# Performance work log

Hardware: AMD Instinct MI355X
Metric: run time of the kernel (lower is better)

The kernel has to match this reference:

```python
import jax, jax.numpy as jnp
import numpy as np

N, F, H, O, L, E = 20000, 256, 256, 128, 3, 320000


def setup_inputs() -> dict:
    key = jax.random.key(0)
    ks = jax.random.split(key, 8)
    x = jax.random.normal(ks[0], (N, F), dtype=jnp.float32)
    edge_index = jax.random.randint(ks[1], (2, E), 0, N, dtype=jnp.int64)
    edge_attributes = jax.random.uniform(ks[2], (E,), dtype=jnp.float32)
    s = 1.0 / np.sqrt(H)
    w_rel = jax.random.uniform(ks[3], (L, H, H), minval=-s, maxval=s, dtype=jnp.float32)
    b_rel = jax.random.uniform(ks[4], (L, H), minval=-s, maxval=s, dtype=jnp.float32)
    w_root = jax.random.uniform(ks[5], (L, H, H), minval=-s, maxval=s, dtype=jnp.float32)
    w_out = jax.random.uniform(ks[6], (H, O), minval=-s, maxval=s, dtype=jnp.float32)
    b_out = jax.random.uniform(ks[7], (O,), minval=-s, maxval=s, dtype=jnp.float32)
    return {"x": x, "edge_index": edge_index, "edge_attributes": edge_attributes,
            "w_rel": w_rel, "b_rel": b_rel, "w_root": w_root,
            "w_out": w_out, "b_out": b_out}


def reference(x, edge_index, edge_attributes, w_rel, b_rel, w_root, w_out, b_out):
    # PyG GraphConv: h_i' = W_root h_i + W_rel (sum_{j->i} e_ji h_j) + b_rel
    src = edge_index[0]  # message source j
    dst = edge_index[1]  # message target i
    n = x.shape[0]
    h = x
    for l in range(w_rel.shape[0]):
        msgs = h[src] * edge_attributes[:, None]            # [E, H] gather + scale
        agg = jax.ops.segment_sum(msgs, dst, num_segments=n)  # [N, H] scatter-add
        h = jax.nn.relu(agg @ w_rel[l] + b_rel[l] + h @ w_root[l])
    return jax.nn.relu(h @ w_out + b_out)  # [N, O]
```

## Files before the change

kernel.cpp:

```cpp
#include <hip/hip_runtime.h>

#define NREAL 20000
#define MPAD  20096
#define HDIM  256
#define ODIM  128
#define NEDGE 320000
#define SCAN_B 20

typedef __attribute__((ext_vector_type(4))) float f32x4;
typedef __attribute__((ext_vector_type(2))) float f32x2;
typedef __attribute__((ext_vector_type(8))) short s16x8;
typedef __attribute__((ext_vector_type(4))) unsigned short u16x4;
typedef unsigned short u16;
typedef unsigned int u32;

__device__ inline u16 f2bf(float f) {
    u32 u = __float_as_uint(f);
    return (u16)((u + 0x7FFFu + ((u >> 16) & 1u)) >> 16);
}
__device__ inline float bf2f(u16 s) { return __uint_as_float(((u32)s) << 16); }

__device__ __forceinline__ void gload16(const void* g, void* l) {
    __builtin_amdgcn_global_load_lds((const __attribute__((address_space(1))) void*)g,
                                     (__attribute__((address_space(3))) void*)l, 16, 0, 0);
}

__global__ __launch_bounds__(256) void k_prep(
    const float* __restrict__ x, u16* __restrict__ hbf,
    const float* __restrict__ wrel, const float* __restrict__ wroot,
    const float* __restrict__ wout,
    u16* __restrict__ brelT, u16* __restrict__ brootT, u16* __restrict__ boutT,
    const int* __restrict__ dst, int* __restrict__ deg)
{
    const int gt = blockIdx.x * 256 + threadIdx.x;
    const int gsz = gridDim.x * 256;
    for (long gid = gt; gid < (long)MPAD * HDIM / 4; gid += gsz) {
        long base = gid * 4;
        long row  = base >> 8;
        f32x4 v = {0.f, 0.f, 0.f, 0.f};
        if (row < NREAL) v = *(const f32x4*)(x + base);
        u16x4 hv;
        for (int j = 0; j < 4; ++j) hv[j] = f2bf(v[j]);
        *(u16x4*)(hbf + base) = hv;
    }
    for (int i = gt; i < 3 * 65536; i += gsz) {
        int l = i >> 16, r = i & 65535, n = r >> 8, k = r & 255;
        brelT[i]  = f2bf(wrel [l * 65536 + k * 256 + n]);
        brootT[i] = f2bf(wroot[l * 65536 + k * 256 + n]);
    }
    for (int i = gt; i < 128 * 256; i += gsz) {
        int n = i >> 8, k = i & 255;
        boutT[i] = f2bf(wout[k * 128 + n]);
    }
    for (int e = gt; e < NEDGE; e += gsz) atomicAdd(&deg[dst[e]], 1);
}

__global__ __launch_bounds__(1024) void k_blocksum(const int* __restrict__ deg,
                                                   int* __restrict__ bsum) {
    __shared__ int red[16];
    int b = blockIdx.x, t = threadIdx.x;
    int i = b * 1024 + t;
    int v = (i < NREAL) ? deg[i] : 0;
    for (int off = 32; off; off >>= 1) v += __shfl_down(v, off);
    if ((t & 63) == 0) red[t >> 6] = v;
    __syncthreads();
    if (t < 16) {
        int s = red[t];
        for (int off = 8; off; off >>= 1) s += __shfl_down(s, off);
        if (t == 0) bsum[b] = s;
    }
}

__global__ void k_scansmall(const int* __restrict__ bsum, int* __restrict__ boff) {
    int t = threadIdx.x;
    int v = (t < SCAN_B) ? bsum[t] : 0;
    int orig = v;
    for (int off = 1; off < 64; off <<= 1) {
        int u = __shfl_up(v, off);
        if (t >= off) v += u;
    }
    if (t < SCAN_B) boff[t] = v - orig;
}

__global__ __launch_bounds__(1024) void k_scanfinal(const int* __restrict__ deg,
                                                    const int* __restrict__ boff,
                                                    int* __restrict__ rowptr,
                                                    int* __restrict__ cursor) {
    __shared__ int sm[1024];
    int b = blockIdx.x, t = threadIdx.x;
    int i = b * 1024 + t;
    int v = (i < NREAL) ? deg[i] : 0;
    sm[t] = v;
    __syncthreads();
    for (int off = 1; off < 1024; off <<= 1) {
        int u = (t >= off) ? sm[t - off] : 0;
        __syncthreads();
        if (t >= off) sm[t] += u;
        __syncthreads();
    }
    if (i < NREAL) {
        int excl = boff[b] + sm[t] - v;
        rowptr[i] = excl;
        cursor[i] = excl;
    }
    if (b == 0 && t == 0) rowptr[NREAL] = NEDGE;
}

__global__ void k_fill(const int* __restrict__ src, const int* __restrict__ dst,
                       const float* __restrict__ attr, int* __restrict__ cursor,
                       u32* __restrict__ csr_edge) {
    int e = blockIdx.x * 256 + threadIdx.x;
    if (e < NEDGE) {
        int d = dst[e];
        int p = atomicAdd(&cursor[d], 1);
        csr_edge[p] = (((u32)f2bf(attr[e])) << 16) | (u32)src[e];
    }
}

__device__ __forceinline__ void agg_pairs(u32 ej, int npair, int half, int col8,
                                          const u16* __restrict__ hbf, f32x2 acc2[4]) {
    const int nbat = (npair + 7) >> 3;
    for (int bt = 0; bt < nbat; ++bt) {
        u32 ee[8];
        s16x8 v[8];
        #pragma unroll
        for (int b = 0; b < 8; ++b) {
            ee[b] = (u32)__shfl((int)ej, 2 * (bt * 8 + b) + half);
            v[b]  = *(const s16x8*)(hbf + ((long)(ee[b] & 0xffffu) << 8) + col8);
        }
        #pragma unroll
        for (int b = 0; b < 8; ++b) {
            float a = __uint_as_float(ee[b] & 0xffff0000u);
            f32x2 a2 = {a, a};
            const u32* vw = (const u32*)&v[b];
            #pragma unroll
            for (int k = 0; k < 4; ++k) {
                f32x2 hv = {__uint_as_float(vw[k] << 16),
                            __uint_as_float(vw[k] & 0xffff0000u)};
                acc2[k] += a2 * hv;
            }
        }
    }
}

template <bool SORT>
__global__ __launch_bounds__(256) void k_aggregate(
    const u16* __restrict__ hbf, const int* __restrict__ rowptr,
    u32* __restrict__ csr_edge, u16* __restrict__ agg)
{
    const int node = blockIdx.x * 4 + (threadIdx.x >> 6);
    const int lane = threadIdx.x & 63;
    const int half = lane >> 5;
    const int col8 = (lane & 31) * 8;
    f32x2 acc2[4];
    #pragma unroll
    for (int k = 0; k < 4; ++k) { acc2[k][0] = 0.f; acc2[k][1] = 0.f; }

    if (node < NREAL) {
        const int beg = rowptr[node], end = rowptr[node + 1];
        const int deg = end - beg;
        bool reg_path = false;
        u32 ej = 0;
        if (SORT) {
            if (deg >= 1 && deg <= 64) {
                u32 val = (lane < deg) ? csr_edge[beg + lane] : 0xFFFFFFFFu;
                if (deg > 1) {
                    #pragma unroll
                    for (int ph = 0; ph < 64; ++ph) {
                        int base = ph & 1;
                        int partner = lane + (((lane ^ base) & 1) ? -1 : +1);
                        if (partner < 0 || partner > 63) partner = lane;
                        u32 p = (u32)__shfl((int)val, partner);
                        if (partner != lane)
                            val = (lane < partner) ? (val < p ? val : p) : (val > p ? val : p);
                    }
                }
                if (lane < deg) csr_edge[beg + lane] = val;
                ej = (lane < deg) ? val : 0u;
                reg_path = true;
            } else if (deg > 64 && lane == 0) {
                for (int i = beg + 1; i < end; ++i) {
                    u32 key = csr_edge[i];
                    int j = i - 1;
                    while (j >= beg && csr_edge[j] > key) { csr_edge[j + 1] = csr_edge[j]; --j; }
                    csr_edge[j + 1] = key;
                }
            }
        }
        if (reg_path) {
            agg_pairs(ej, (deg + 1) >> 1, half, col8, hbf, acc2);
        } else {
            for (int c = beg; c < end; c += 64) {
                int m = end - c; if (m > 64) m = 64;
                u32 ejc = csr_edge[c + (lane < m ? lane : 0)];
                if (lane >= m) ejc = 0u;
                agg_pairs(ejc, (m + 1) >> 1, half, col8, hbf, acc2);
            }
        }
    }
    #pragma unroll
    for (int k = 0; k < 4; ++k) {
        acc2[k][0] += __shfl_xor(acc2[k][0], 32);
        acc2[k][1] += __shfl_xor(acc2[k][1], 32);
    }
    if (half == 0) {
        s16x8 hv;
        #pragma unroll
        for (int k = 0; k < 4; ++k) {
            hv[2 * k]     = (short)f2bf(acc2[k][0]);
            hv[2 * k + 1] = (short)f2bf(acc2[k][1]);
        }
        *(s16x8*)(agg + (long)node * HDIM + col8) = hv;
    }
}

__global__ __launch_bounds__(256) void k_gemm(
    const u16* __restrict__ A1, const u16* __restrict__ A2,
    const u16* __restrict__ BT1, const u16* __restrict__ BT2,
    const float* __restrict__ bias,
    u16* __restrict__ hout, float* __restrict__ final_out, int Nt)
{
    __shared__ __align__(16) u16 As[64 * 64];
    __shared__ __align__(16) u16 Bs[128 * 64];

    const int t    = threadIdx.x;
    const int bm   = blockIdx.x, bn = blockIdx.y;
    const int lane = t & 63;
    const int wave = t >> 6;
    const int wr   = (wave >> 1) * 32;
    const int wc   = (wave & 1) * 64;
    const int lrow = lane & 15;
    const int lks  = lane >> 4;

    f32x4 acc[2][4];
    #pragma unroll
    for (int i = 0; i < 2; ++i)
        #pragma unroll
        for (int j = 0; j < 4; ++j)
            #pragma unroll
            for (int r = 0; r < 4; ++r) acc[i][j][r] = 0.f;

    const int lrow8 = lane >> 3;
    const int ssrc  = ((lane & 7) ^ lrow8) * 8;

    const int nmat = A2 ? 2 : 1;
    for (int mat = 0; mat < nmat; ++mat) {
        const u16* A_g = mat ? A2  : A1;
        const u16* B_g = mat ? BT2 : BT1;
        for (int k0 = 0; k0 < HDIM; k0 += 64) {
            __syncthreads();
            #pragma unroll
            for (int i = 0; i < 2; ++i) {
                int ch  = wave * 2 + i;
                int row = ch * 8 + lrow8;
                gload16(A_g + (size_t)(bm * 64 + row) * HDIM + k0 + ssrc, &As[ch * 512]);
            }
            #pragma unroll
            for (int i = 0; i < 4; ++i) {
                int ch  = wave * 4 + i;
                int row = ch * 8 + lrow8;
                gload16(B_g + (size_t)(bn * 128 + row) * HDIM + k0 + ssrc, &Bs[ch * 512]);
            }
            __syncthreads();
            #pragma unroll
            for (int kk = 0; kk < 2; ++kk) {
                int slot = kk * 4 + lks;
                s16x8 bfr[4];
                #pragma unroll
                for (int nj = 0; nj < 4; ++nj) {
                    int r = wc + nj * 16 + lrow;
                    bfr[nj] = *(const s16x8*)&Bs[r * 64 + ((slot ^ (r & 7)) * 8)];
                }
                #pragma unroll
                for (int mi = 0; mi < 2; ++mi) {
                    int r = wr + mi * 16 + lrow;
                    s16x8 a = *(const s16x8*)&As[r * 64 + ((slot ^ (r & 7)) * 8)];
                    #pragma unroll
                    for (int nj = 0; nj < 4; ++nj)
                        acc[mi][nj] = __builtin_amdgcn_mfma_f32_16x16x32_bf16(a, bfr[nj], acc[mi][nj], 0, 0, 0);
                }
            }
        }
    }

    const int rb = (lane >> 4) * 4;
    #pragma unroll
    for (int mi = 0; mi < 2; ++mi) {
        #pragma unroll
        for (int nj = 0; nj < 4; ++nj) {
            int col = bn * 128 + wc + nj * 16 + lrow;
            float bsv = bias[col];
            #pragma unroll
            for (int r = 0; r < 4; ++r) {
                int row = bm * 64 + wr + mi * 16 + rb + r;
                float v = acc[mi][nj][r] + bsv;
                v = v > 0.f ? v : 0.f;
                if (final_out) {
                    if (row < NREAL) final_out[(long)row * Nt + col] = v;
                } else {
                    hout[(long)row * HDIM + col] = f2bf(v);
                }
            }
        }
    }
}

static inline char* align256(char* p) {
    return (char*)(((size_t)p + 255) & ~(size_t)255);
}

extern "C" void kernel_launch(void* const* d_in, const int* in_sizes, int n_in,
                              void* d_out, int out_size, void* d_ws, size_t ws_size,
                              hipStream_t stream) {
    const float* x     = (const float*)d_in[0];
    const int*   eidx  = (const int*)  d_in[1];
    const float* attr  = (const float*)d_in[2];
    const float* wrel  = (const float*)d_in[3];
    const float* brel  = (const float*)d_in[4];
    const float* wroot = (const float*)d_in[5];
    const float* wout  = (const float*)d_in[6];
    const float* bout  = (const float*)d_in[7];
    const int* src = eidx;
    const int* dst = eidx + NEDGE;

    char* ws = (char*)d_ws;
    u16* hbfA  = (u16*)ws;        ws = align256(ws + (size_t)MPAD * HDIM * 2);
    u16* hbfB  = (u16*)ws;        ws = align256(ws + (size_t)MPAD * HDIM * 2);
    u16* aggbf = (u16*)ws;        ws = align256(ws + (size_t)MPAD * HDIM * 2);
    u16* brelT  = (u16*)ws;       ws = align256(ws + (size_t)3 * 65536 * 2);
    u16* brootT = (u16*)ws;       ws = align256(ws + (size_t)3 * 65536 * 2);
    u16* boutT  = (u16*)ws;       ws = align256(ws + (size_t)128 * 256 * 2);
    int* deg    = (int*)ws;       ws = align256(ws + (size_t)NREAL * 4);
    int* rowptr = (int*)ws;       ws = align256(ws + (size_t)(NREAL + 1) * 4);
    int* cursor = (int*)ws;       ws = align256(ws + (size_t)NREAL * 4);
    int* bsum   = (int*)ws;       ws = align256(ws + (size_t)SCAN_B * 4);
    int* boff   = (int*)ws;       ws = align256(ws + (size_t)SCAN_B * 4);
    u32* csr_edge = (u32*)ws;     ws = align256(ws + (size_t)NEDGE * 4);

    hipMemsetAsync(deg, 0, (size_t)NREAL * 4, stream);
    k_prep<<<2048, 256, 0, stream>>>(x, hbfA, wrel, wroot, wout,
                                     brelT, brootT, boutT, dst, deg);
    k_blocksum<<<SCAN_B, 1024, 0, stream>>>(deg, bsum);
    k_scansmall<<<1, 64, 0, stream>>>(bsum, boff);
    k_scanfinal<<<SCAN_B, 1024, 0, stream>>>(deg, boff, rowptr, cursor);
    k_fill<<<(NEDGE + 255) / 256, 256, 0, stream>>>(src, dst, attr, cursor, csr_edge);

    u16* h_c = hbfA;
    u16* h_n = hbfB;
    for (int l = 0; l < 3; ++l) {
        if (l == 0)
            k_aggregate<true><<<MPAD / 4, 256, 0, stream>>>(h_c, rowptr, csr_edge, aggbf);
        else
            k_aggregate<false><<<MPAD / 4, 256, 0, stream>>>(h_c, rowptr, csr_edge, aggbf);
        k_gemm<<<dim3(MPAD / 64, 2), 256, 0, stream>>>(
            aggbf, h_c,
            brelT + (size_t)l * 65536, brootT + (size_t)l * 65536,
            brel + (size_t)l * HDIM,
            h_n, nullptr, HDIM);
        u16* tp = h_c; h_c = h_n; h_n = tp;
    }
    k_gemm<<<dim3(MPAD / 64, 1), 256, 0, stream>>>(
        h_c, nullptr, boutT, nullptr, bout,
        nullptr, (float*)d_out, ODIM);
}
```

Before: 169.5 us.

## Process two nodes per wave in aggregation and fold small scan into final scan

Each aggregation wave now handles two nodes (n and n+MPAD/2), loading both rowptr ranges and edge lists up front so the memory latency of the second node overlaps the first. Grid size is halved to match. The tiny block-offset scan kernel is removed and recomputed redundantly inside each final-scan block, saving one launch. This trades per-wave parallelism and occupancy for more loads in flight, and a deg>64 path in the sort variant now waits explicitly on memory.

```diff
diff --git a/kernel.cpp b/kernel.cpp
--- a/kernel.cpp
+++ b/kernel.cpp
@@ -71,23 +71,22 @@
     }
 }
 
-__global__ void k_scansmall(const int* __restrict__ bsum, int* __restrict__ boff) {
-    int t = threadIdx.x;
-    int v = (t < SCAN_B) ? bsum[t] : 0;
-    int orig = v;
-    for (int off = 1; off < 64; off <<= 1) {
-        int u = __shfl_up(v, off);
-        if (t >= off) v += u;
-    }
-    if (t < SCAN_B) boff[t] = v - orig;
-}
-
 __global__ __launch_bounds__(1024) void k_scanfinal(const int* __restrict__ deg,
-                                                    const int* __restrict__ boff,
+                                                    const int* __restrict__ bsum,
                                                     int* __restrict__ rowptr,
                                                     int* __restrict__ cursor) {
     __shared__ int sm[1024];
+    __shared__ int chunkoff;
     int b = blockIdx.x, t = threadIdx.x;
+    if (t < 64) {
+        int v = (t < SCAN_B) ? bsum[t] : 0;
+        int orig = v;
+        for (int off = 1; off < 64; off <<= 1) {
+            int u = __shfl_up(v, off);
+            if (t >= off) v += u;
+        }
+        if (t == b) chunkoff = v - orig;
+    }
     int i = b * 1024 + t;
     int v = (i < NREAL) ? deg[i] : 0;
     sm[t] = v;
@@ -99,7 +98,7 @@
         __syncthreads();
     }
     if (i < NREAL) {
-        int excl = boff[b] + sm[t] - v;
+        int excl = chunkoff + sm[t] - v;
         rowptr[i] = excl;
         cursor[i] = excl;
     }
@@ -144,26 +143,20 @@
 }
 
 template <bool SORT>
-__global__ __launch_bounds__(256) void k_aggregate(
-    const u16* __restrict__ hbf, const int* __restrict__ rowptr,
-    u32* __restrict__ csr_edge, u16* __restrict__ agg)
+__device__ __forceinline__ void do_node(
+    int node, int beg, int deg, u32 ejf,
+    int lane, int half, int col8,
+    const u16* __restrict__ hbf, u32* __restrict__ csr_edge,
+    u16* __restrict__ agg)
 {
-    const int node = blockIdx.x * 4 + (threadIdx.x >> 6);
-    const int lane = threadIdx.x & 63;
-    const int half = lane >> 5;
-    const int col8 = (lane & 31) * 8;
     f32x2 acc2[4];
     #pragma unroll
     for (int k = 0; k < 4; ++k) { acc2[k][0] = 0.f; acc2[k][1] = 0.f; }
 
     if (node < NREAL) {
-        const int beg = rowptr[node], end = rowptr[node + 1];
-        const int deg = end - beg;
-        bool reg_path = false;
-        u32 ej = 0;
-        if (SORT) {
-            if (deg >= 1 && deg <= 64) {
-                u32 val = (lane < deg) ? csr_edge[beg + lane] : 0xFFFFFFFFu;
+        if (deg >= 1 && deg <= 64) {
+            u32 val = ejf;
+            if (SORT) {
                 if (deg > 1) {
                     #pragma unroll
                     for (int ph = 0; ph < 64; ++ph) {
@@ -176,22 +169,23 @@
                     }
                 }
                 if (lane < deg) csr_edge[beg + lane] = val;
-                ej = (lane < deg) ? val : 0u;
-                reg_path = true;
-            } else if (deg > 64 && lane == 0) {
-                for (int i = beg + 1; i < end; ++i) {
-                    u32 key = csr_edge[i];
-                    int j = i - 1;
-                    while (j >= beg && csr_edge[j] > key) { csr_edge[j + 1] = csr_edge[j]; --j; }
-                    csr_edge[j + 1] = key;
-                }
-            }
-        }
-        if (reg_path) {
-            agg_pairs(ej, (deg + 1) >> 1, half, col8, hbf, acc2);
-        } else {
-            for (int c = beg; c < end; c += 64) {
-                int m = end - c; if (m > 64) m = 64;
+                else            val = 0u;
+            }
+            agg_pairs(val, (deg + 1) >> 1, half, col8, hbf, acc2);
+        } else if (deg > 64) {
+            if (SORT) {
+                if (lane == 0) {
+                    for (int i = beg + 1; i < beg + deg; ++i) {
+                        u32 key = csr_edge[i];
+                        int j = i - 1;
+                        while (j >= beg && csr_edge[j] > key) { csr_edge[j + 1] = csr_edge[j]; --j; }
+                        csr_edge[j + 1] = key;
+                    }
+                }
+                asm volatile("s_waitcnt vmcnt(0)" ::: "memory");
+            }
+            for (int c = beg; c < beg + deg; c += 64) {
+                int m = beg + deg - c; if (m > 64) m = 64;
                 u32 ejc = csr_edge[c + (lane < m ? lane : 0)];
                 if (lane >= m) ejc = 0u;
                 agg_pairs(ejc, (m + 1) >> 1, half, col8, hbf, acc2);
@@ -212,6 +206,29 @@
         }
         *(s16x8*)(agg + (long)node * HDIM + col8) = hv;
     }
+}
+
+template <bool SORT>
+__global__ __launch_bounds__(256) void k_aggregate(
+    const u16* __restrict__ hbf, const int* __restrict__ rowptr,
+    u32* __restrict__ csr_edge, u16* __restrict__ agg)
+{
+    const int lane = threadIdx.x & 63;
+    const int half = lane >> 5;
+    const int col8 = (lane & 31) * 8;
+    const int n0 = blockIdx.x * 4 + (threadIdx.x >> 6);
+    const int n1 = n0 + MPAD / 2;
+
+    int beg0 = 0, deg0 = 0, beg1 = 0, deg1 = 0;
+    if (n0 < NREAL) { beg0 = rowptr[n0]; deg0 = rowptr[n0 + 1] - beg0; }
+    if (n1 < NREAL) { beg1 = rowptr[n1]; deg1 = rowptr[n1 + 1] - beg1; }
+    u32 ej0 = SORT ? 0xFFFFFFFFu : 0u;
+    u32 ej1 = SORT ? 0xFFFFFFFFu : 0u;
+    if (deg0 >= 1 && deg0 <= 64 && lane < deg0) ej0 = csr_edge[beg0 + lane];
+    if (deg1 >= 1 && deg1 <= 64 && lane < deg1) ej1 = csr_edge[beg1 + lane];
+
+    do_node<SORT>(n0, beg0, deg0, ej0, lane, half, col8, hbf, csr_edge, agg);
+    do_node<SORT>(n1, beg1, deg1, ej1, lane, half, col8, hbf, csr_edge, agg);
 }
 
 __global__ __launch_bounds__(256) void k_gemm(
@@ -334,24 +351,22 @@
     int* rowptr = (int*)ws;       ws = align256(ws + (size_t)(NREAL + 1) * 4);
     int* cursor = (int*)ws;       ws = align256(ws + (size_t)NREAL * 4);
     int* bsum   = (int*)ws;       ws = align256(ws + (size_t)SCAN_B * 4);
-    int* boff   = (int*)ws;       ws = align256(ws + (size_t)SCAN_B * 4);
     u32* csr_edge = (u32*)ws;     ws = align256(ws + (size_t)NEDGE * 4);
 
     hipMemsetAsync(deg, 0, (size_t)NREAL * 4, stream);
     k_prep<<<2048, 256, 0, stream>>>(x, hbfA, wrel, wroot, wout,
                                      brelT, brootT, boutT, dst, deg);
     k_blocksum<<<SCAN_B, 1024, 0, stream>>>(deg, bsum);
-    k_scansmall<<<1, 64, 0, stream>>>(bsum, boff);
-    k_scanfinal<<<SCAN_B, 1024, 0, stream>>>(deg, boff, rowptr, cursor);
+    k_scanfinal<<<SCAN_B, 1024, 0, stream>>>(deg, bsum, rowptr, cursor);
     k_fill<<<(NEDGE + 255) / 256, 256, 0, stream>>>(src, dst, attr, cursor, csr_edge);
 
     u16* h_c = hbfA;
     u16* h_n = hbfB;
     for (int l = 0; l < 3; ++l) {
         if (l == 0)
-            k_aggregate<true><<<MPAD / 4, 256, 0, stream>>>(h_c, rowptr, csr_edge, aggbf);
+            k_aggregate<true><<<MPAD / 8, 256, 0, stream>>>(h_c, rowptr, csr_edge, aggbf);
         else
-            k_aggregate<false><<<MPAD / 4, 256, 0, stream>>>(h_c, rowptr, csr_edge, aggbf);
+            k_aggregate<false><<<MPAD / 8, 256, 0, stream>>>(h_c, rowptr, csr_edge, aggbf);
         k_gemm<<<dim3(MPAD / 64, 2), 256, 0, stream>>>(
             aggbf, h_c,
             brelT + (size_t)l * 65536, brootT + (size_t)l * 65536,
```

Measured after the change: 171.0 us. Within noise of the previous version (+0.9%).
